# Kernel optimization log

Hardware: AMD Instinct MI355X
Metric: run time of the kernel (lower is better)

The kernel has to match this reference:

```python
import jax, jax.numpy as jnp
import numpy as np

N_HEAD = 16


def _rope_tables(T, head_dim, dtype):
    # RotaryEmbedding buffers: freqs = outer(t, inv_freq), half-dim tables [T, head_dim//2]
    inv_freq = 1.0 / (10000.0 ** (jnp.arange(0, head_dim, 2, dtype=jnp.float32) / head_dim))
    freqs = jnp.arange(T, dtype=jnp.float32)[:, None] * inv_freq[None, :]
    return jnp.cos(freqs).astype(dtype), jnp.sin(freqs).astype(dtype)


def _apply_rotary(x, cos, sin):
    # x: [B,H,T,D]; cos/sin: [T,D//2] broadcast over B,H
    d = x.shape[-1] // 2
    x1, x2 = x[..., :d], x[..., d:]
    return jnp.concatenate([x1 * cos - x2 * sin, x2 * cos + x1 * sin], axis=-1)


def setup_inputs() -> dict:
    key = jax.random.key(0)
    k1, k2, k3 = jax.random.split(key, 3)
    B, T, C = 2, 2048, 2048
    x = jax.random.normal(k1, (B, T, C), dtype=jnp.float32)
    Wqkv = jax.random.normal(k2, (C, 3 * C), dtype=jnp.float32) * (1.0 / np.sqrt(C))
    Wproj = jax.random.normal(k3, (C, C), dtype=jnp.float32) * (1.0 / np.sqrt(C))
    return {"x": x, "Wqkv": Wqkv, "Wproj": Wproj}


def reference(x, Wqkv, Wproj):
    B, T, C = x.shape
    H = N_HEAD
    D = C // H
    qkv = (x @ Wqkv).reshape(B, T, 3, H, D)
    q, k, v = qkv[:, :, 0], qkv[:, :, 1], qkv[:, :, 2]  # [B,T,H,D]
    q = jnp.transpose(q, (0, 2, 1, 3))  # [B,H,T,D]
    k = jnp.transpose(k, (0, 2, 1, 3))
    v = jnp.transpose(v, (0, 2, 1, 3))
    cos, sin = _rope_tables(T, D, x.dtype)
    q = _apply_rotary(q, cos, sin)
    k = _apply_rotary(k, cos, sin)
    scale = 1.0 / np.sqrt(D)
    scores = jnp.einsum('bhqd,bhkd->bhqk', q, k) * scale
    causal = jnp.tril(jnp.ones((T, T), dtype=bool))
    scores = jnp.where(causal, scores, jnp.finfo(scores.dtype).min)
    attn = jax.nn.softmax(scores, axis=-1)
    out = jnp.einsum('bhqk,bhkd->bhqd', attn, v)
    out = jnp.transpose(out, (0, 2, 1, 3)).reshape(B, T, C)
    return out @ Wproj
```

## Files before the change

kernel.cpp:

```cpp
#include <hip/hip_runtime.h>
#include <hip/hip_bf16.h>

typedef short s16b;
using bf16x4 = __attribute__((ext_vector_type(4))) short;
using bf16x8 = __attribute__((ext_vector_type(8))) short;
using f32x4  = __attribute__((ext_vector_type(4))) float;

#define DEVINL __device__ __forceinline__

DEVINL float bf2f(short u) {
    union { float f; unsigned u; } x;
    x.u = ((unsigned)(unsigned short)u) << 16;
    return x.f;
}
DEVINL short f2bf(float f) {
    unsigned u = __builtin_bit_cast(unsigned, f);
    u += 0x7FFFu + ((u >> 16) & 1u);
    return (short)(u >> 16);
}

DEVINL f32x4 mfma16(bf16x8 a, bf16x8 b, f32x4 c) {
    return __builtin_amdgcn_mfma_f32_16x16x32_bf16(a, b, c, 0, 0, 0);
}

DEVINL void gload_lds16(const void* g, void* lds_uniform) {
    __builtin_amdgcn_global_load_lds(
        (const __attribute__((address_space(1))) char*)(const char*)g,
        (__attribute__((address_space(3))) char*)(char*)lds_uniform, 16, 0, 0);
}

DEVINL int perm32(int k) {
    return ((k >> 2) & 3) * 8 + ((k >> 4) & 1) * 4 + (k & 3);
}

DEVINL bf16x8 lds128(const s16b* base, int row, int ks, int g) {
    const char* p = (const char*)base + row * 128 + ((((ks << 2) + g) ^ (row & 7)) << 4);
    return *(const bf16x8*)p;
}
DEVINL bf16x8 lds256(const s16b* base, int row, int ds, int g) {
    const char* p = (const char*)base + row * 256 + ((((ds << 2) + g) ^ (row & 7)) << 4);
    return *(const bf16x8*)p;
}

__global__ void k_tables(float* __restrict__ ctab, float* __restrict__ stab) {
    int idx = blockIdx.x * 256 + threadIdx.x;
    int i = idx & 63, t = idx >> 6;
    float inv = powf(10000.0f, -(float)i * (1.0f / 64.0f));
    float fr = (float)t * inv;
    ctab[idx] = cosf(fr);
    stab[idx] = sinf(fr);
}

__global__ void k_cvt_x(const float* __restrict__ x, s16b* __restrict__ xb) {
    int idx = blockIdx.x * 256 + threadIdx.x;
    int p = idx * 4;
    int row = p >> 11, pc = p & 2047;
    int grp = pc >> 5, sp = pc & 31;
    int c = sp >> 3, half = (sp >> 2) & 1;
    int ksrc = grp * 32 + half * 16 + c * 4;
    float4 v = *(const float4*)(x + (size_t)row * 2048 + ksrc);
    bf16x4 o;
    o[0] = f2bf(v.x); o[1] = f2bf(v.y); o[2] = f2bf(v.z); o[3] = f2bf(v.w);
    *(bf16x4*)(xb + (size_t)row * 2048 + pc) = o;
}

__global__ void k_tcvt(const float* __restrict__ in, s16b* __restrict__ out, int R, int C) {
    __shared__ float tile[32][33];
    int tx = threadIdx.x & 31, ty = threadIdx.x >> 5;
    int c0 = blockIdx.x * 32, r0 = blockIdx.y * 32;
#pragma unroll
    for (int kk = 0; kk < 4; ++kk) {
        int r = ty + kk * 8;
        tile[r][tx] = in[(size_t)(r0 + r) * C + c0 + tx];
    }
    __syncthreads();
#pragma unroll
    for (int kk = 0; kk < 4; ++kk) {
        int r = ty + kk * 8;
        out[(size_t)(c0 + r) * R + r0 + perm32(tx)] = f2bf(tile[tx][r]);
    }
}

#define STG_A(H, KB, DB)                                                       \
  gload_lds16(srcA + (H) * 262144 + (KB), lds + (DB) * 16384 + (H) * 8192 + wave * 1024);
#define STG_B(H, KB, DB)                                                       \
  gload_lds16(srcB + (H) * 524288 + (KB),                                      \
              lds + 32768 + (DB) * 32768 + (H) * 16384 + wave * 1024);         \
  gload_lds16(srcB + (H) * 524288 + 262144 + (KB),                             \
              lds + 32768 + (DB) * 32768 + (H) * 16384 + 8192 + wave * 1024);

#define AF_READ(BUF, KS)                                                       \
    _Pragma("unroll")                                                          \
    for (int fi = 0; fi < 4; ++fi) {                                           \
      int row = (fi >> 1) * 64 + wm * 32 + (fi & 1) * 16 + r15;                \
      af[fi] = *(const bf16x8*)(lds + (BUF) * 16384 + row * 128                \
               + ((((KS) * 4 + g) ^ (row & 7)) << 4));                         \
    }
#define BF_READ(BUF, KS, BH)                                                   \
    _Pragma("unroll")                                                          \
    for (int fj = 0; fj < 2; ++fj) {                                           \
      int row = (BH) * 128 + wn * 32 + fj * 16 + r15;                          \
      bfr[fj] = *(const bf16x8*)(lds + 32768 + (BUF) * 32768 + row * 128       \
                + ((((KS) * 4 + g) ^ (row & 7)) << 4));                        \
    }

#define PH(BUF, KS, BH, NEWA, STGC, WAITN)                                     \
  {                                                                            \
    if (NEWA) AF_READ(BUF, KS)                                                 \
    BF_READ(BUF, KS, BH)                                                       \
    STGC                                                                       \
    if ((WAITN) == 2) { asm volatile("s_waitcnt vmcnt(2)" ::: "memory");       \
                        __builtin_amdgcn_sched_barrier(0); }                   \
    else if ((WAITN) == 0) { asm volatile("s_waitcnt vmcnt(0)" ::: "memory");  \
                        __builtin_amdgcn_sched_barrier(0); }                   \
    asm volatile("s_waitcnt lgkmcnt(0)" ::: "memory");                         \
    __builtin_amdgcn_sched_barrier(0);                                         \
    __builtin_amdgcn_s_barrier();                                              \
    __builtin_amdgcn_sched_barrier(0);                                         \
    __builtin_amdgcn_s_setprio(1);                                             \
    _Pragma("unroll")                                                          \
    for (int fi = 0; fi < 4; ++fi)                                             \
      _Pragma("unroll")                                                        \
      for (int fj = 0; fj < 2; ++fj)                                           \
        acc[fi][(BH) * 2 + fj] = mfma16(af[fi], bfr[fj], acc[fi][(BH) * 2 + fj]); \
    __builtin_amdgcn_s_setprio(0);                                             \
  }

#define GEMM8_MAINLOOP(A_, B_)                                                 \
    __shared__ __attribute__((aligned(16))) char lds[98304];                   \
    const int tid = threadIdx.x;                                               \
    const int lane = tid & 63, wave = tid >> 6;                                \
    const int g = lane >> 4, r15 = lane & 15;                                  \
    const int wm = wave >> 2, wn = wave & 3;                                   \
    const int lin = wave * 1024 + (lane << 4);                                 \
    const int rowL = lin >> 7;                                                 \
    const int swzL = ((((lin >> 4) & 7) ^ (rowL & 7)) << 4);                   \
    const char* srcA = (const char*)(A_) + (size_t)(bm + rowL) * 4096 + swzL;  \
    const char* srcB = (const char*)(B_) + (size_t)(bn + rowL) * 4096 + swzL;  \
    f32x4 acc[4][4] = {};                                                      \
    bf16x8 af[4], bfr[2];                                                      \
    STG_B(0, 0, 0) STG_A(0, 0, 0) STG_A(1, 0, 0) STG_B(1, 0, 0)                \
    asm volatile("s_waitcnt vmcnt(2)" ::: "memory");                           \
    __builtin_amdgcn_sched_barrier(0);                                         \
    __builtin_amdgcn_s_barrier();                                              \
    for (int t2 = 0; t2 < 15; ++t2) {                                          \
        const int kb1 = t2 * 256 + 128, kb2 = t2 * 256 + 256;                  \
        PH(0, 0, 0, 1, STG_B(0, kb1, 1), 2)                                    \
        PH(0, 0, 1, 0, STG_A(0, kb1, 1), -1)                                   \
        PH(0, 1, 0, 1, STG_A(1, kb1, 1), -1)                                   \
        PH(0, 1, 1, 0, STG_B(1, kb1, 1), 2)                                    \
        PH(1, 0, 0, 1, STG_B(0, kb2, 0), 2)                                    \
        PH(1, 0, 1, 0, STG_A(0, kb2, 0), -1)                                   \
        PH(1, 1, 0, 1, STG_A(1, kb2, 0), -1)                                   \
        PH(1, 1, 1, 0, STG_B(1, kb2, 0), 2)                                    \
    }                                                                          \
    PH(0, 0, 0, 1, STG_B(0, 3968, 1), 2)                                       \
    PH(0, 0, 1, 0, STG_A(0, 3968, 1), -1)                                      \
    PH(0, 1, 0, 1, STG_A(1, 3968, 1), -1)                                      \
    PH(0, 1, 1, 0, STG_B(1, 3968, 1), 2)                                       \
    PH(1, 0, 0, 1, , 0)                                                        \
    PH(1, 0, 1, 0, , -1)                                                       \
    PH(1, 1, 0, 1, , -1)                                                       \
    PH(1, 1, 1, 0, , -1)

__global__ __launch_bounds__(512) void k_gemm_qkv(
    const s16b* __restrict__ A, const s16b* __restrict__ Bt,
    s16b* __restrict__ Qb, s16b* __restrict__ Kb, s16b* __restrict__ Vt) {
    const int bid = blockIdx.x;
    const int sbid = (bid & 7) * 96 + (bid >> 3);
    const int bm = (sbid / 24) * 128, bn = (sbid % 24) * 256;
    GEMM8_MAINLOOP(A, Bt)
#pragma unroll
    for (int i = 0; i < 4; ++i) {
        int m0 = bm + (i >> 1) * 64 + wm * 32 + (i & 1) * 16 + 4 * g;
        int b = m0 >> 11, t0 = m0 & 2047;
#pragma unroll
        for (int j = 0; j < 4; ++j) {
            int n = bn + (j >> 1) * 128 + wn * 32 + (j & 1) * 16 + r15;
            int which = n >> 11;
            int h = (n >> 7) & 15, d = n & 127;
            size_t bh = (size_t)(b * 16 + h);
            if (which == 0) {
                size_t base = (bh * 2048 + t0) * 128 + d;
#pragma unroll
                for (int e = 0; e < 4; ++e) Qb[base + (size_t)e * 128] = f2bf(acc[i][j][e]);
            } else if (which == 1) {
                size_t base = (bh * 2048 + t0) * 128 + d;
#pragma unroll
                for (int e = 0; e < 4; ++e) Kb[base + (size_t)e * 128] = f2bf(acc[i][j][e]);
            } else {
                int pt = (t0 & ~31) + perm32(t0 & 31);
                size_t base = (bh * 128 + d) * 2048 + pt;
                bf16x4 pk;
#pragma unroll
                for (int e = 0; e < 4; ++e) pk[e] = f2bf(acc[i][j][e]);
                *(bf16x4*)(Vt + base) = pk;
            }
        }
    }
}

__global__ __launch_bounds__(512) void k_gemm_proj(
    const s16b* __restrict__ A, const s16b* __restrict__ Bt, float* __restrict__ Co) {
    const int bid = blockIdx.x;
    const int sbid = (bid & 7) * 32 + (bid >> 3);
    const int bm = (sbid / 8) * 128, bn = (sbid % 8) * 256;
    GEMM8_MAINLOOP(A, Bt)
#pragma unroll
    for (int i = 0; i < 4; ++i) {
        int m0 = bm + (i >> 1) * 64 + wm * 32 + (i & 1) * 16 + 4 * g;
#pragma unroll
        for (int j = 0; j < 4; ++j) {
            int n = bn + (j >> 1) * 128 + wn * 32 + (j & 1) * 16 + r15;
#pragma unroll
            for (int e = 0; e < 4; ++e) Co[(size_t)(m0 + e) * 2048 + n] = acc[i][j][e];
        }
    }
}

__global__ void k_rope(s16b* __restrict__ Qb, const s16b* __restrict__ Kb,
                       s16b* __restrict__ Kp,
                       const float* __restrict__ ctab, const float* __restrict__ stab) {
    int idx = blockIdx.x * 256 + threadIdx.x;
    int i4 = idx & 15;
    int t = (idx >> 4) & 2047;
    int bh = (idx >> 15) & 31;
    int which = idx >> 20;
    int d = i4 * 4;
    const float* cp = ctab + t * 64 + d;
    const float* sp = stab + t * 64 + d;
    size_t rowoff = ((size_t)bh * 2048 + t) * 128;
    if (which == 0) {
        s16b* P = Qb + rowoff;
        bf16x4 a = *(bf16x4*)(P + d);
        bf16x4 bv = *(bf16x4*)(P + d + 64);
        bf16x4 ra, rb;
#pragma unroll
        for (int e = 0; e < 4; ++e) {
            float c = cp[e], s = sp[e];
            float x1 = bf2f(a[e]), x2 = bf2f(bv[e]);
            ra[e] = f2bf(x1 * c - x2 * s);
            rb[e] = f2bf(x2 * c + x1 * s);
        }
        *(bf16x4*)(P + d) = ra;
        *(bf16x4*)(P + d + 64) = rb;
    } else {
        const s16b* Pi = Kb + rowoff;
        s16b* Po = Kp + rowoff;
        bf16x4 a = *(const bf16x4*)(Pi + d);
        bf16x4 bv = *(const bf16x4*)(Pi + d + 64);
        bf16x4 ra, rb;
#pragma unroll
        for (int e = 0; e < 4; ++e) {
            float c = cp[e], s = sp[e];
            float x1 = bf2f(a[e]), x2 = bf2f(bv[e]);
            ra[e] = f2bf(x1 * c - x2 * s);
            rb[e] = f2bf(x2 * c + x1 * s);
        }
        int d2 = d + 64;
        int pd  = (d  & ~31) + perm32(d  & 31);
        int pd2 = (d2 & ~31) + perm32(d2 & 31);
        *(bf16x4*)(Po + pd) = ra;
        *(bf16x4*)(Po + pd2) = rb;
    }
}

__global__ __launch_bounds__(256) void k_attn(
    const s16b* __restrict__ Qb, const s16b* __restrict__ Kp,
    const s16b* __restrict__ Vt, s16b* __restrict__ AO) {
    __shared__ alignas(16) s16b Ks[64 * 128];
    __shared__ alignas(16) s16b Vs[128 * 64];
    const int tid = threadIdx.x;
    const int lane = tid & 63, wave = tid >> 6;
    const int g = lane >> 4, r15 = lane & 15;
    const int bh = blockIdx.x, qt = 15 - blockIdx.y;
    const int q0 = qt * 128 + wave * 32;
    const s16b* Qg = Qb + (size_t)bh * 2048 * 128;
    const char* Kg = (const char*)(Kp + (size_t)bh * 2048 * 128);
    const char* Vg = (const char*)(Vt + (size_t)bh * 128 * 2048);

    bf16x8 qf[2][4];
#pragma unroll
    for (int qs = 0; qs < 2; ++qs)
#pragma unroll
        for (int ds = 0; ds < 4; ++ds) {
            const s16b* p = Qg + (size_t)(q0 + qs * 16 + r15) * 128 + ds * 32 + 4 * g;
            bf16x4 lo = *(const bf16x4*)p;
            bf16x4 hi = *(const bf16x4*)(p + 16);
            qf[qs][ds] = __builtin_shufflevector(lo, hi, 0, 1, 2, 3, 4, 5, 6, 7);
        }

    f32x4 ot[8][2] = {};
    float m_s[2] = {-3e38f, -3e38f};
    float l_s[2] = {0.f, 0.f};
    const float scale = 0.0883883476483184f;

    const int ktiles = qt * 2 + 2;
    for (int kt = 0; kt < ktiles; ++kt) {
        const int k0 = kt * 64;
        __syncthreads();
#pragma unroll
        for (int rr = 0; rr < 4; ++rr) {
            int uo = (rr * 256 + wave * 64) * 16;
            int o = uo + lane * 16;
            {
                int row = o >> 8, sl = (o >> 4) & 15;
                int sg = (sl ^ (row & 7)) << 4;
                gload_lds16(Kg + (size_t)(k0 + row) * 256 + sg, (char*)Ks + uo);
            }
            {
                int row = o >> 7, sl = (o >> 4) & 7;
                int sg = (sl ^ (row & 7)) << 4;
                gload_lds16(Vg + (size_t)row * 4096 + (size_t)k0 * 2 + sg, (char*)Vs + uo);
            }
        }
        __syncthreads();

        if (k0 <= q0 + 31) {
            f32x4 st[4][2] = {};
            __builtin_amdgcn_s_setprio(1);
#pragma unroll
            for (int ds = 0; ds < 4; ++ds) {
#pragma unroll
                for (int ks = 0; ks < 4; ++ks) {
                    bf16x8 kf = lds256(Ks, ks * 16 + r15, ds, g);
#pragma unroll
                    for (int qs = 0; qs < 2; ++qs)
                        st[ks][qs] = mfma16(kf, qf[qs][ds], st[ks][qs]);
                }
            }
            __builtin_amdgcn_s_setprio(0);
#pragma unroll
            for (int ks = 0; ks < 4; ++ks)
#pragma unroll
                for (int qs = 0; qs < 2; ++qs)
#pragma unroll
                    for (int e = 0; e < 4; ++e) {
                        int kk = k0 + ks * 16 + 4 * g + e;
                        int qq = q0 + qs * 16 + r15;
                        float s = st[ks][qs][e] * scale;
                        st[ks][qs][e] = (kk <= qq) ? s : -3e38f;
                    }
            float sf[2];
#pragma unroll
            for (int qs = 0; qs < 2; ++qs) {
                float mx = -3e38f;
#pragma unroll
                for (int ks = 0; ks < 4; ++ks)
#pragma unroll
                    for (int e = 0; e < 4; ++e) mx = fmaxf(mx, st[ks][qs][e]);
                mx = fmaxf(mx, __shfl_xor(mx, 16));
                mx = fmaxf(mx, __shfl_xor(mx, 32));
                float mn = fmaxf(m_s[qs], mx);
                sf[qs] = __expf(m_s[qs] - mn);
                m_s[qs] = mn;
                float sum = 0.f;
#pragma unroll
                for (int ks = 0; ks < 4; ++ks)
#pragma unroll
                    for (int e = 0; e < 4; ++e) {
                        float p = __expf(st[ks][qs][e] - mn);
                        st[ks][qs][e] = p;
                        sum += p;
                    }
                sum += __shfl_xor(sum, 16);
                sum += __shfl_xor(sum, 32);
                l_s[qs] = l_s[qs] * sf[qs] + sum;
            }
            bf16x8 pb[2][2];
#pragma unroll
            for (int k2 = 0; k2 < 2; ++k2)
#pragma unroll
                for (int qs = 0; qs < 2; ++qs) {
                    bf16x8 f;
#pragma unroll
                    for (int jj = 0; jj < 8; ++jj)
                        f[jj] = f2bf(st[2 * k2 + (jj >> 2)][qs][jj & 3]);
                    pb[k2][qs] = f;
                }
#pragma unroll
            for (int d8 = 0; d8 < 8; ++d8)
#pragma unroll
                for (int qs = 0; qs < 2; ++qs)
#pragma unroll
                    for (int e = 0; e < 4; ++e) ot[d8][qs][e] *= sf[qs];
            __builtin_amdgcn_s_setprio(1);
#pragma unroll
            for (int k2 = 0; k2 < 2; ++k2)
#pragma unroll
                for (int d8 = 0; d8 < 8; ++d8) {
                    bf16x8 vf = lds128(Vs, d8 * 16 + r15, k2, g);
#pragma unroll
                    for (int qs = 0; qs < 2; ++qs)
                        ot[d8][qs] = mfma16(vf, pb[k2][qs], ot[d8][qs]);
                }
            __builtin_amdgcn_s_setprio(0);
        }
    }
    int b = bh >> 4, h = bh & 15;
#pragma unroll
    for (int qs = 0; qs < 2; ++qs) {
        float inv = 1.0f / l_s[qs];
        int q = q0 + qs * 16 + r15;
#pragma unroll
        for (int d8 = 0; d8 < 8; ++d8) {
            bf16x4 pk;
#pragma unroll
            for (int e = 0; e < 4; ++e) pk[e] = f2bf(ot[d8][qs][e] * inv);
            size_t off = ((size_t)(b * 2048 + q)) * 2048
                       + h * 128 + (d8 >> 1) * 32 + g * 8 + (d8 & 1) * 4;
            *(bf16x4*)(AO + off) = pk;
        }
    }
}

extern "C" void kernel_launch(void* const* d_in, const int* in_sizes, int n_in,
                              void* d_out, int out_size, void* d_ws, size_t ws_size,
                              hipStream_t stream) {
    const float* x = (const float*)d_in[0];
    const float* Wqkv = (const float*)d_in[1];
    const float* Wproj = (const float*)d_in[2];
    float* out = (float*)d_out;

    char* ws = (char*)d_ws;
    float* ctab = (float*)ws;
    float* stab = ctab + 2048 * 64;
    size_t off = 1048576;
    s16b* xb = (s16b*)(ws + off); off += 16777216;
    s16b* wqkvt = (s16b*)(ws + off); off += 25165824;
    s16b* wprojt = (s16b*)(ws + off); off += 8388608;
    s16b* Qb = (s16b*)(ws + off); off += 16777216;
    s16b* Kb = (s16b*)(ws + off); off += 16777216;
    s16b* Vt = (s16b*)(ws + off); off += 16777216;
    s16b* AO = xb;
    s16b* Kp = wqkvt;

    k_tables<<<dim3(512), dim3(256), 0, stream>>>(ctab, stab);
    k_cvt_x<<<dim3(8192), dim3(256), 0, stream>>>(x, xb);
    k_tcvt<<<dim3(192, 64), dim3(256), 0, stream>>>(Wqkv, wqkvt, 2048, 6144);
    k_tcvt<<<dim3(64, 64), dim3(256), 0, stream>>>(Wproj, wprojt, 2048, 2048);
    k_gemm_qkv<<<dim3(768), dim3(512), 0, stream>>>(xb, wqkvt, Qb, Kb, Vt);
    k_rope<<<dim3(8192), dim3(256), 0, stream>>>(Qb, Kb, Kp, ctab, stab);
    k_attn<<<dim3(32, 16), dim3(256), 0, stream>>>(Qb, Kp, Vt, AO);
    k_gemm_proj<<<dim3(256), dim3(512), 0, stream>>>(AO, wprojt, out);
}
```

Measured before the change: 277.1 us.

## Triple-buffer GEMM mainloop with one barrier per K tile and XCD-aware tiling

Replaces the double-buffered, eight-phase GEMM mainloop with a triple-buffered one. Each K tile is staged with six global-to-LDS loads issued together and two K-substeps of 16 MFMAs, with a single barrier per tile instead of one per phase. Block-to-tile mapping is also changed so each XCD gets a contiguous 2D region of output tiles, improving L2 reuse of A and B. LDS usage rises from 96KB to 144KB, and the vmcnt accounting changes, so prefetch correctness depends on the wait counts being right.

```diff
diff --git a/kernel.cpp b/kernel.cpp
--- a/kernel.cpp
+++ b/kernel.cpp
@@ -81,95 +81,90 @@
     }
 }
 
-#define STG_A(H, KB, DB)                                                       \
-  gload_lds16(srcA + (H) * 262144 + (KB), lds + (DB) * 16384 + (H) * 8192 + wave * 1024);
-#define STG_B(H, KB, DB)                                                       \
-  gload_lds16(srcB + (H) * 524288 + (KB),                                      \
-              lds + 32768 + (DB) * 32768 + (H) * 16384 + wave * 1024);         \
-  gload_lds16(srcB + (H) * 524288 + 262144 + (KB),                             \
-              lds + 32768 + (DB) * 32768 + (H) * 16384 + 8192 + wave * 1024);
-
-#define AF_READ(BUF, KS)                                                       \
+#define STG_TILE(DB, KB)                                                       \
+  gload_lds16(srcA + (KB), lds + (DB) * 16384 + tid16);                        \
+  gload_lds16(srcA + 262144 + (KB), lds + (DB) * 16384 + 8192 + tid16);        \
+  gload_lds16(srcB + (KB), lds + 49152 + (DB) * 32768 + tid16);                \
+  gload_lds16(srcB + 262144 + (KB), lds + 49152 + (DB) * 32768 + 8192 + tid16);\
+  gload_lds16(srcB + 524288 + (KB), lds + 49152 + (DB) * 32768 + 16384 + tid16);\
+  gload_lds16(srcB + 786432 + (KB), lds + 49152 + (DB) * 32768 + 24576 + tid16);
+
+#define AF_READ(B, KS)                                                         \
     _Pragma("unroll")                                                          \
     for (int fi = 0; fi < 4; ++fi) {                                           \
       int row = (fi >> 1) * 64 + wm * 32 + (fi & 1) * 16 + r15;                \
-      af[fi] = *(const bf16x8*)(lds + (BUF) * 16384 + row * 128                \
+      af[fi] = *(const bf16x8*)(lds + (B) * 16384 + row * 128                  \
                + ((((KS) * 4 + g) ^ (row & 7)) << 4));                         \
     }
-#define BF_READ(BUF, KS, BH)                                                   \
+#define BF_READ(B, KS)                                                         \
     _Pragma("unroll")                                                          \
-    for (int fj = 0; fj < 2; ++fj) {                                           \
-      int row = (BH) * 128 + wn * 32 + fj * 16 + r15;                          \
-      bfr[fj] = *(const bf16x8*)(lds + 32768 + (BUF) * 32768 + row * 128       \
+    for (int fj = 0; fj < 4; ++fj) {                                           \
+      int row = (fj >> 1) * 128 + wn * 32 + (fj & 1) * 16 + r15;               \
+      bfr[fj] = *(const bf16x8*)(lds + 49152 + (B) * 32768 + row * 128         \
                 + ((((KS) * 4 + g) ^ (row & 7)) << 4));                        \
     }
 
-#define PH(BUF, KS, BH, NEWA, STGC, WAITN)                                     \
+#define MFMAS                                                                  \
+  __builtin_amdgcn_s_setprio(1);                                               \
+  _Pragma("unroll")                                                            \
+  for (int fi = 0; fi < 4; ++fi)                                               \
+    _Pragma("unroll")                                                          \
+    for (int fj = 0; fj < 4; ++fj)                                             \
+      acc[fi][fj] = mfma16(af[fi], bfr[fj], acc[fi][fj]);                      \
+  __builtin_amdgcn_s_setprio(0);
+
+#define DO_TILE(B, B2, KB, DOSTG, WN)                                          \
   {                                                                            \
-    if (NEWA) AF_READ(BUF, KS)                                                 \
-    BF_READ(BUF, KS, BH)                                                       \
-    STGC                                                                       \
-    if ((WAITN) == 2) { asm volatile("s_waitcnt vmcnt(2)" ::: "memory");       \
-                        __builtin_amdgcn_sched_barrier(0); }                   \
-    else if ((WAITN) == 0) { asm volatile("s_waitcnt vmcnt(0)" ::: "memory");  \
-                        __builtin_amdgcn_sched_barrier(0); }                   \
-    asm volatile("s_waitcnt lgkmcnt(0)" ::: "memory");                         \
+    AF_READ(B, 0) BF_READ(B, 0)                                                \
+    if (DOSTG) { STG_TILE(B2, (KB) + 256) }                                    \
+    MFMAS                                                                      \
+    AF_READ(B, 1) BF_READ(B, 1)                                                \
+    if ((WN) == 6) { asm volatile("s_waitcnt vmcnt(6)" ::: "memory");          \
+                     __builtin_amdgcn_sched_barrier(0); }                      \
+    else if ((WN) == 0) { asm volatile("s_waitcnt vmcnt(0)" ::: "memory");     \
+                     __builtin_amdgcn_sched_barrier(0); }                      \
+    MFMAS                                                                      \
+    __builtin_amdgcn_s_barrier();                                              \
+    asm volatile("" ::: "memory");                                             \
     __builtin_amdgcn_sched_barrier(0);                                         \
-    __builtin_amdgcn_s_barrier();                                              \
-    __builtin_amdgcn_sched_barrier(0);                                         \
-    __builtin_amdgcn_s_setprio(1);                                             \
-    _Pragma("unroll")                                                          \
-    for (int fi = 0; fi < 4; ++fi)                                             \
-      _Pragma("unroll")                                                        \
-      for (int fj = 0; fj < 2; ++fj)                                           \
-        acc[fi][(BH) * 2 + fj] = mfma16(af[fi], bfr[fj], acc[fi][(BH) * 2 + fj]); \
-    __builtin_amdgcn_s_setprio(0);                                             \
   }
 
-#define GEMM8_MAINLOOP(A_, B_)                                                 \
-    __shared__ __attribute__((aligned(16))) char lds[98304];                   \
+#define GEMM3_MAINLOOP(A_, B_)                                                 \
+    __shared__ __attribute__((aligned(16))) char lds[147456];                  \
     const int tid = threadIdx.x;                                               \
     const int lane = tid & 63, wave = tid >> 6;                                \
     const int g = lane >> 4, r15 = lane & 15;                                  \
     const int wm = wave >> 2, wn = wave & 3;                                   \
-    const int lin = wave * 1024 + (lane << 4);                                 \
-    const int rowL = lin >> 7;                                                 \
-    const int swzL = ((((lin >> 4) & 7) ^ (rowL & 7)) << 4);                   \
+    const int tid16 = tid << 4;                                                \
+    const int rowL = tid16 >> 7;                                               \
+    const int swzL = ((((tid16 >> 4) & 7) ^ (rowL & 7)) << 4);                 \
     const char* srcA = (const char*)(A_) + (size_t)(bm + rowL) * 4096 + swzL;  \
     const char* srcB = (const char*)(B_) + (size_t)(bn + rowL) * 4096 + swzL;  \
     f32x4 acc[4][4] = {};                                                      \
-    bf16x8 af[4], bfr[2];                                                      \
-    STG_B(0, 0, 0) STG_A(0, 0, 0) STG_A(1, 0, 0) STG_B(1, 0, 0)                \
-    asm volatile("s_waitcnt vmcnt(2)" ::: "memory");                           \
+    bf16x8 af[4], bfr[4];                                                      \
+    STG_TILE(0, 0) STG_TILE(1, 128)                                            \
+    asm volatile("s_waitcnt vmcnt(6)" ::: "memory");                           \
     __builtin_amdgcn_sched_barrier(0);                                         \
     __builtin_amdgcn_s_barrier();                                              \
-    for (int t2 = 0; t2 < 15; ++t2) {                                          \
-        const int kb1 = t2 * 256 + 128, kb2 = t2 * 256 + 256;                  \
-        PH(0, 0, 0, 1, STG_B(0, kb1, 1), 2)                                    \
-        PH(0, 0, 1, 0, STG_A(0, kb1, 1), -1)                                   \
-        PH(0, 1, 0, 1, STG_A(1, kb1, 1), -1)                                   \
-        PH(0, 1, 1, 0, STG_B(1, kb1, 1), 2)                                    \
-        PH(1, 0, 0, 1, STG_B(0, kb2, 0), 2)                                    \
-        PH(1, 0, 1, 0, STG_A(0, kb2, 0), -1)                                   \
-        PH(1, 1, 0, 1, STG_A(1, kb2, 0), -1)                                   \
-        PH(1, 1, 1, 0, STG_B(1, kb2, 0), 2)                                    \
+    asm volatile("" ::: "memory");                                             \
+    for (int t3 = 0; t3 < 10; ++t3) {                                          \
+        const int kb = t3 * 384;                                               \
+        DO_TILE(0, 2, kb, 1, 6)                                                \
+        DO_TILE(1, 0, kb + 128, 1, 6)                                          \
+        DO_TILE(2, 1, kb + 256, 1, 6)                                          \
     }                                                                          \
-    PH(0, 0, 0, 1, STG_B(0, 3968, 1), 2)                                       \
-    PH(0, 0, 1, 0, STG_A(0, 3968, 1), -1)                                      \
-    PH(0, 1, 0, 1, STG_A(1, 3968, 1), -1)                                      \
-    PH(0, 1, 1, 0, STG_B(1, 3968, 1), 2)                                       \
-    PH(1, 0, 0, 1, , 0)                                                        \
-    PH(1, 0, 1, 0, , -1)                                                       \
-    PH(1, 1, 0, 1, , -1)                                                       \
-    PH(1, 1, 1, 0, , -1)
+    DO_TILE(0, 2, 3840, 0, 0)                                                  \
+    DO_TILE(1, 0, 3968, 0, -1)
 
 __global__ __launch_bounds__(512) void k_gemm_qkv(
     const s16b* __restrict__ A, const s16b* __restrict__ Bt,
     s16b* __restrict__ Qb, s16b* __restrict__ Kb, s16b* __restrict__ Vt) {
     const int bid = blockIdx.x;
-    const int sbid = (bid & 7) * 96 + (bid >> 3);
-    const int bm = (sbid / 24) * 128, bn = (sbid % 24) * 256;
-    GEMM8_MAINLOOP(A, Bt)
+    const int xcd = bid & 7, local = bid >> 3;
+    const int rr_ = local >> 5, w = local & 31;
+    const int bm = ((xcd & 3) * 8 + (w >> 2)) * 128;
+    const int bn = ((xcd >> 2) * 12 + rr_ * 4 + (w & 3)) * 256;
+    GEMM3_MAINLOOP(A, Bt)
 #pragma unroll
     for (int i = 0; i < 4; ++i) {
         int m0 = bm + (i >> 1) * 64 + wm * 32 + (i & 1) * 16 + 4 * g;
@@ -203,9 +198,10 @@
 __global__ __launch_bounds__(512) void k_gemm_proj(
     const s16b* __restrict__ A, const s16b* __restrict__ Bt, float* __restrict__ Co) {
     const int bid = blockIdx.x;
-    const int sbid = (bid & 7) * 32 + (bid >> 3);
-    const int bm = (sbid / 8) * 128, bn = (sbid % 8) * 256;
-    GEMM8_MAINLOOP(A, Bt)
+    const int xcd = bid & 7, local = bid >> 3;
+    const int bm = (xcd * 4 + (local & 3)) * 128;
+    const int bn = (local >> 2) * 256;
+    GEMM3_MAINLOOP(A, Bt)
 #pragma unroll
     for (int i = 0; i < 4; ++i) {
         int m0 = bm + (i >> 1) * 64 + wm * 32 + (i & 1) * 16 + 4 * g;
```

Measured after the change: 273.1 us. About the same (-1.4%).
